# Optimization experiments

Hardware: AMD Instinct MI355X
Metric: run time of the kernel (lower is better)

The kernel has to match this reference:

```python
import jax, jax.numpy as jnp
import numpy as np

SIGMA = 0.01        # config['fscore_sigma']
FSCORE_W = 0.1      # config['fscore_weight']
TASK_W = 1.0        # config['task_weight']
DOMAIN_W = 0.1      # config['domain_weight']


def setup_inputs() -> dict:
    key = jax.random.key(0)
    ks = jax.random.split(key, 11)
    B, N, M, F = 8, 4096, 4096, 512
    H1, H2, D = 256, 128, 6
    return {
        "pred_pc": jax.random.normal(ks[0], (B, N, 3), jnp.float32),
        "target_pc": jax.random.normal(ks[1], (B, M, 3), jnp.float32),
        "domain_features": jax.random.normal(ks[2], (B, F), jnp.float32),
        "dataset_weights": jax.random.uniform(ks[3], (B,), jnp.float32, 0.9, 1.2),
        "W1": jax.random.normal(ks[4], (F, H1), jnp.float32) * 0.02,
        "b1": jnp.zeros((H1,), jnp.float32),
        "W2": jax.random.normal(ks[5], (H1, H2), jnp.float32) * 0.02,
        "b2": jnp.zeros((H2,), jnp.float32),
        "W3": jax.random.normal(ks[6], (H2, D), jnp.float32) * 0.02,
        "b3": jnp.zeros((D,), jnp.float32),
        "domain_labels": jax.random.randint(ks[7], (B,), 0, D),
    }


def _chamfer_mins(pred, tgt):
    # pred: [B,N,3], tgt: [B,M,3] -> squared pairwise dists [B,N,M], then dual mins
    d = (jnp.sum(pred ** 2, axis=2)[:, :, None]
         + jnp.sum(tgt ** 2, axis=2)[:, None, :]
         - 2.0 * jnp.einsum('bnd,bmd->bnm', pred, tgt))
    return jnp.min(d, axis=2), jnp.min(d, axis=1)   # [B,N], [B,M]


def reference(pred_pc, target_pc, domain_features, dataset_weights,
              W1, b1, W2, b2, W3, b3, domain_labels):
    min_a, min_b = _chamfer_mins(pred_pc, target_pc)
    c = 2.0 * SIGMA * SIGMA
    soft_a = jnp.exp(-min_a / c)
    soft_b = jnp.exp(-min_b / c)

    # batch-level task loss (compute_reconstruction_loss on full batch)
    chamfer = jnp.mean(min_a) + jnp.mean(min_b)
    prec = jnp.mean(soft_a)
    rec = jnp.mean(soft_b)
    fscore = 2.0 * prec * rec / (prec + rec + 1e-8)
    task = chamfer + FSCORE_W * (1.0 - fscore)

    # per-sample dataset-weighted loss (vectorized form of the Python loop)
    ch_i = jnp.mean(min_a, axis=1) + jnp.mean(min_b, axis=1)
    p_i = jnp.mean(soft_a, axis=1)
    r_i = jnp.mean(soft_b, axis=1)
    f_i = 2.0 * p_i * r_i / (p_i + r_i + 1e-8)
    loss_i = ch_i + FSCORE_W * (1.0 - f_i)
    dataset_weighted = jnp.mean(dataset_weights * loss_i)

    # domain loss: GRL is identity in forward; classifier in eval mode (dropout off)
    h = jax.nn.relu(domain_features @ W1 + b1)
    h = jax.nn.relu(h @ W2 + b2)
    logits = h @ W3 + b3
    logp = jax.nn.log_softmax(logits, axis=-1)
    domain = -jnp.mean(jnp.take_along_axis(logp, domain_labels[:, None], axis=1))

    total = TASK_W * task + DOMAIN_W * domain + dataset_weighted
    return total
```

## Files before the change

kernel.cpp:

```cpp
#include <hip/hip_runtime.h>
#include <math.h>

#define B 8
#define NPTS 4096
#define QPT 8
#define THREADS 256


template<int S, int LOG2S>
__global__ __launch_bounds__(THREADS, 4) void d1_kernel(
    const float* __restrict__ pred, const float* __restrict__ targ,
    const float* __restrict__ x, const float* __restrict__ W1,
    float* __restrict__ partial, float* __restrict__ sums32,
    float* __restrict__ h1p) {
  constexpr int REFS = NPTS / S;
  int id = blockIdx.x;
  int tid = threadIdx.x;

  __shared__ float4 refs[REFS];
  __shared__ float xs[64];

  if (id < 64) {
    if (id == 0 && tid < 32) sums32[tid] = 0.f;
    int b = id >> 3, kc = id & 7;
    if (tid < 64) xs[tid] = x[b * 512 + kc * 64 + tid];
    __syncthreads();
    float acc = 0.f;
    const float* w = W1 + (size_t)(kc * 64) * 256 + tid;
#pragma unroll 8
    for (int k = 0; k < 64; ++k) acc = fmaf(xs[k], w[k * 256], acc);
    h1p[(b * 8 + kc) * 256 + tid] = acc;
    return;
  }

  int cid = id - 64;
  int split  = cid & (S - 1);
  int qchunk = (cid >> LOG2S) & 1;
  int b      = (cid >> (LOG2S + 1)) & 7;
  int dir    = cid >> (LOG2S + 4);
  const float* qp = dir ? targ : pred;
  const float* rp = dir ? pred : targ;

  const float* rb = rp + ((size_t)b * NPTS + (size_t)split * REFS) * 3;
  for (int i = tid; i < REFS; i += THREADS) {
    float xx = rb[i * 3 + 0], yy = rb[i * 3 + 1], zz = rb[i * 3 + 2];
    refs[i] = make_float4(xx, yy, zz, 0.5f * (xx * xx + yy * yy + zz * zz));
  }
  __syncthreads();

  const float* qb = qp + (size_t)b * NPTS * 3;
  int q0 = qchunk * (QPT * THREADS) + tid;
  float qx[QPT], qy[QPT], qz[QPT], vmin[QPT];
#pragma unroll
  for (int i = 0; i < QPT; ++i) {
    int q = q0 + i * THREADS;
    qx[i] = qb[q * 3 + 0];
    qy[i] = qb[q * 3 + 1];
    qz[i] = qb[q * 3 + 2];
    vmin[i] = 3.4e38f;
  }

  for (int j = 0; j < REFS; j += 8) {
    float4 t[8];
#pragma unroll
    for (int u = 0; u < 8; ++u) t[u] = refs[j + u];
#pragma unroll
    for (int i = 0; i < QPT; ++i) {
      float s[8];
#pragma unroll
      for (int u = 0; u < 8; ++u)
        s[u] = fmaf(-qx[i], t[u].x,
               fmaf(-qy[i], t[u].y, fmaf(-qz[i], t[u].z, t[u].w)));
      float m01 = fminf(s[0], s[1]), m23 = fminf(s[2], s[3]);
      float m45 = fminf(s[4], s[5]), m67 = fminf(s[6], s[7]);
      vmin[i] = fminf(vmin[i],
                      fminf(fminf(m01, m23), fminf(m45, m67)));
    }
  }

  size_t base = (((size_t)dir * B + b) * S + split) * NPTS;
#pragma unroll
  for (int i = 0; i < QPT; ++i) {
    float qn = fmaf(qx[i], qx[i], fmaf(qy[i], qy[i], qz[i] * qz[i]));
    partial[base + q0 + i * THREADS] = fmaf(2.f, vmin[i], qn);
  }
}

template<int S>
__global__ __launch_bounds__(THREADS) void d2_kernel(
    const float* __restrict__ partial, float* __restrict__ sums32,
    const float* __restrict__ h1p, const float* __restrict__ b1,
    const float* __restrict__ W2, float* __restrict__ h2p) {
  int id = blockIdx.x;
  int tid = threadIdx.x;

  if (id >= 256) {
    int lid = id - 256;
    int b = lid >> 1, half = lid & 1;
    __shared__ float hs[128];
    if (tid < 128) {
      int k = half * 128 + tid;
      float a = b1[k];
#pragma unroll
      for (int p = 0; p < 8; ++p) a += h1p[(b * 8 + p) * 256 + k];
      hs[tid] = fmaxf(a, 0.f);
    }
    __syncthreads();
    if (tid < 128) {
      float acc = 0.f;
      const float* w = W2 + (size_t)(half * 128) * 128 + tid;
#pragma unroll 8
      for (int k = 0; k < 128; ++k) acc = fmaf(hs[k], w[k * 128], acc);
      h2p[(b * 2 + half) * 128 + tid] = acc;
    }
    return;
  }

  int chunk = id & 15;
  int b   = (id >> 4) & 7;
  int dir = id >> 7;
  size_t pb = ((size_t)dir * B + b) * S * NPTS;
  int q = chunk * 256 + tid;

  float m = 3.4e38f;
#pragma unroll
  for (int s = 0; s < S; ++s)
    m = fminf(m, partial[pb + (size_t)s * NPTS + q]);
  float s_min = m;
  float s_soft = __expf(-5000.0f * m);

  for (int off = 32; off > 0; off >>= 1) {
    s_min  += __shfl_down(s_min,  off);
    s_soft += __shfl_down(s_soft, off);
  }
  __shared__ float red[8];
  int wave = tid >> 6, lane = tid & 63;
  if (lane == 0) { red[wave * 2] = s_min; red[wave * 2 + 1] = s_soft; }
  __syncthreads();
  if (tid == 0) {
    float a = 0.f, c = 0.f;
    for (int w = 0; w < 4; ++w) { a += red[w * 2]; c += red[w * 2 + 1]; }
    atomicAdd(&sums32[(dir * B + b) * 2 + 0], a);
    atomicAdd(&sums32[(dir * B + b) * 2 + 1], c);
  }
}

__global__ __launch_bounds__(THREADS) void final_kernel(
    const float* __restrict__ h2p, const float* __restrict__ b2,
    const float* __restrict__ W3, const float* __restrict__ b3,
    const int* __restrict__ labels, const float* __restrict__ sums32,
    const float* __restrict__ w, float* __restrict__ out) {
  int tid = threadIdx.x;
  __shared__ float h2s[8 * 128];
  __shared__ float lg[48];
  __shared__ float nlls[8];

  for (int i = tid; i < 1024; i += THREADS) {
    int b = i >> 7, j = i & 127;
    float a = b2[j] + h2p[(b * 2 + 0) * 128 + j] + h2p[(b * 2 + 1) * 128 + j];
    h2s[i] = fmaxf(a, 0.f);
  }
  __syncthreads();
  if (tid < 48) {
    int b = tid / 6, d = tid % 6;
    float acc = b3[d];
#pragma unroll 8
    for (int k = 0; k < 128; ++k) acc = fmaf(h2s[b * 128 + k], W3[k * 6 + d], acc);
    lg[tid] = acc;
  }
  __syncthreads();
  if (tid < 8) {
    int b = tid;
    float mx = lg[b * 6];
    for (int d = 1; d < 6; ++d) mx = fmaxf(mx, lg[b * 6 + d]);
    float se = 0.f;
    for (int d = 0; d < 6; ++d) se += __expf(lg[b * 6 + d] - mx);
    int lab = labels[b];
    nlls[b] = -(lg[b * 6 + lab] - mx - __logf(se));
  }
  __syncthreads();
  if (tid == 0) {
    float chamfer = 0.f, prec = 0.f, rec = 0.f, dsw = 0.f, dom = 0.f;
    for (int b = 0; b < B; ++b) {
      float sa  = sums32[(0 * B + b) * 2 + 0];
      float ssa = sums32[(0 * B + b) * 2 + 1];
      float sb  = sums32[(1 * B + b) * 2 + 0];
      float ssb = sums32[(1 * B + b) * 2 + 1];
      float ma = sa / 4096.f, mb = sb / 4096.f;
      float p = ssa / 4096.f, r = ssb / 4096.f;
      chamfer += ma + mb;
      prec += p; rec += r;
      float f_i = 2.f * p * r / (p + r + 1e-8f);
      float loss_i = ma + mb + 0.1f * (1.f - f_i);
      dsw += w[b] * loss_i;
      dom += nlls[b];
    }
    chamfer *= (1.f / B); prec *= (1.f / B); rec *= (1.f / B);
    dsw *= (1.f / B); dom *= (1.f / B);
    float fscore = 2.f * prec * rec / (prec + rec + 1e-8f);
    float task = chamfer + 0.1f * (1.f - fscore);
    out[0] = 1.0f * task + 0.1f * dom + dsw;
  }
}

template<int S, int LOG2S>
static void run_pipeline(const float* pred, const float* targ, const float* x,
                         const float* wgt, const float* W1, const float* b1,
                         const float* W2, const float* b2, const float* W3,
                         const float* b3, const int* labels, float* out,
                         char* ws, hipStream_t stream) {
  float* partial = (float*)ws;
  float* sums32  = partial + (size_t)2 * B * S * NPTS;
  float* h1p     = sums32 + 32;
  float* h2p     = h1p + 64 * 256;

  hipLaunchKernelGGL((d1_kernel<S, LOG2S>), dim3(64 + 32 * S), dim3(THREADS),
                     0, stream, pred, targ, x, W1, partial, sums32, h1p);
  hipLaunchKernelGGL((d2_kernel<S>), dim3(256 + 16), dim3(THREADS), 0, stream,
                     partial, sums32, h1p, b1, W2, h2p);
  hipLaunchKernelGGL(final_kernel, dim3(1), dim3(THREADS), 0, stream,
                     h2p, b2, W3, b3, labels, sums32, wgt, out);
}

extern "C" void kernel_launch(void* const* d_in, const int* in_sizes, int n_in,
                              void* d_out, int out_size, void* d_ws, size_t ws_size,
                              hipStream_t stream) {
  const float* pred   = (const float*)d_in[0];
  const float* targ   = (const float*)d_in[1];
  const float* x      = (const float*)d_in[2];
  const float* wgt    = (const float*)d_in[3];
  const float* W1     = (const float*)d_in[4];
  const float* b1     = (const float*)d_in[5];
  const float* W2     = (const float*)d_in[6];
  const float* b2     = (const float*)d_in[7];
  const float* W3     = (const float*)d_in[8];
  const float* b3     = (const float*)d_in[9];
  const int*   labels = (const int*)d_in[10];
  float* out = (float*)d_out;
  char* ws = (char*)d_ws;

  auto need = [](int S) {
    return ((size_t)2 * B * S * NPTS + 32 + 64 * 256 + 16 * 128) * sizeof(float);
  };
  if (ws_size >= need(32))
    run_pipeline<32, 5>(pred, targ, x, wgt, W1, b1, W2, b2, W3, b3, labels,
                        out, ws, stream);
  else if (ws_size >= need(16))
    run_pipeline<16, 4>(pred, targ, x, wgt, W1, b1, W2, b2, W3, b3, labels,
                        out, ws, stream);
  else
    run_pipeline<8, 3>(pred, targ, x, wgt, W1, b1, W2, b2, W3, b3, labels,
                       out, ws, stream);
}
```

Baseline: 111.6 us.

## Fuse three-kernel pipeline into one cooperative persistent kernel with grid syncs

Merges the chamfer-min, reduction and classifier-head kernels into one cooperative kernel. Blocks loop over the old work ids, and grid.sync() replaces the kernel boundaries, which removes two launch gaps. The inner min tree now uses three-input min helpers, which may map to v_min3. Risks: the persistent grid (up to 1024 blocks) may leave the compute phase unbalanced, since 32*S work items are spread over fewer blocks. Grid sync has its own cost, and the extra shared memory may lower occupancy.

Measured after the change: 221.4 us. +98.3%, slower.

```diff
diff --git a/kernel.cpp b/kernel.cpp
--- a/kernel.cpp
+++ b/kernel.cpp
@@ -1,11 +1,213 @@
 #include <hip/hip_runtime.h>
+#include <hip/hip_cooperative_groups.h>
 #include <math.h>
+
+namespace cg = cooperative_groups;
 
 #define B 8
 #define NPTS 4096
 #define QPT 8
 #define THREADS 256
 
+__device__ __forceinline__ float min3f(float a, float b, float c) {
+  return fminf(fminf(a, b), c);
+}
+
+
+template<int S, int LOG2S>
+__global__ __launch_bounds__(THREADS, 4) void fused_kernel(
+    const float* __restrict__ pred, const float* __restrict__ targ,
+    const float* __restrict__ x, const float* __restrict__ W1,
+    const float* __restrict__ b1, const float* __restrict__ W2,
+    const float* __restrict__ b2, const float* __restrict__ W3,
+    const float* __restrict__ b3, const int* __restrict__ labels,
+    const float* __restrict__ wgt,
+    float* __restrict__ partial, float* __restrict__ sums32,
+    float* __restrict__ h1p, float* __restrict__ h2p,
+    float* __restrict__ out) {
+  constexpr int REFS = NPTS / S;
+  cg::grid_group grid = cg::this_grid();
+  const int tid = threadIdx.x;
+
+  __shared__ float4 refs[REFS];
+  __shared__ float xs[64];
+  __shared__ float hs[128];
+  __shared__ float red[8];
+  __shared__ float h2s[8 * 128];
+  __shared__ float lg[48];
+  __shared__ float nlls[8];
+
+  for (int id = blockIdx.x; id < 64; id += gridDim.x) {
+    if (id == 0 && tid < 32) sums32[tid] = 0.f;
+    int b = id >> 3, kc = id & 7;
+    if (tid < 64) xs[tid] = x[b * 512 + kc * 64 + tid];
+    __syncthreads();
+    float acc = 0.f;
+    const float* w = W1 + (size_t)(kc * 64) * 256 + tid;
+#pragma unroll 8
+    for (int k = 0; k < 64; ++k) acc = fmaf(xs[k], w[k * 256], acc);
+    h1p[(b * 8 + kc) * 256 + tid] = acc;
+    __syncthreads();
+  }
+
+  for (int cid = blockIdx.x; cid < 32 * S; cid += gridDim.x) {
+    int split  = cid & (S - 1);
+    int qchunk = (cid >> LOG2S) & 1;
+    int b      = (cid >> (LOG2S + 1)) & 7;
+    int dir    = cid >> (LOG2S + 4);
+    const float* qp = dir ? targ : pred;
+    const float* rp = dir ? pred : targ;
+
+    const float* rb = rp + ((size_t)b * NPTS + (size_t)split * REFS) * 3;
+    for (int i = tid; i < REFS; i += THREADS) {
+      float xx = rb[i * 3 + 0], yy = rb[i * 3 + 1], zz = rb[i * 3 + 2];
+      refs[i] = make_float4(xx, yy, zz, 0.5f * (xx * xx + yy * yy + zz * zz));
+    }
+    __syncthreads();
+
+    const float* qb = qp + (size_t)b * NPTS * 3;
+    int q0 = qchunk * (QPT * THREADS) + tid;
+    float qx[QPT], qy[QPT], qz[QPT], vmin[QPT];
+#pragma unroll
+    for (int i = 0; i < QPT; ++i) {
+      int q = q0 + i * THREADS;
+      qx[i] = qb[q * 3 + 0];
+      qy[i] = qb[q * 3 + 1];
+      qz[i] = qb[q * 3 + 2];
+      vmin[i] = 3.4e38f;
+    }
+
+    for (int j = 0; j < REFS; j += 8) {
+      float4 t[8];
+#pragma unroll
+      for (int u = 0; u < 8; ++u) t[u] = refs[j + u];
+#pragma unroll
+      for (int i = 0; i < QPT; ++i) {
+        float s[8];
+#pragma unroll
+        for (int u = 0; u < 8; ++u)
+          s[u] = fmaf(-qx[i], t[u].x,
+                 fmaf(-qy[i], t[u].y, fmaf(-qz[i], t[u].z, t[u].w)));
+        float m0 = min3f(s[0], s[1], s[2]);
+        float m1 = min3f(s[3], s[4], s[5]);
+        float m2 = min3f(s[6], s[7], m0);
+        vmin[i] = min3f(m1, m2, vmin[i]);
+      }
+    }
+
+    size_t base = (((size_t)dir * B + b) * S + split) * NPTS;
+#pragma unroll
+    for (int i = 0; i < QPT; ++i) {
+      float qn = fmaf(qx[i], qx[i], fmaf(qy[i], qy[i], qz[i] * qz[i]));
+      partial[base + q0 + i * THREADS] = fmaf(2.f, vmin[i], qn);
+    }
+    __syncthreads();
+  }
+
+  grid.sync();
+
+  for (int id = blockIdx.x; id < 272; id += gridDim.x) {
+    if (id >= 256) {
+      int lid = id - 256;
+      int b = lid >> 1, half = lid & 1;
+      if (tid < 128) {
+        int k = half * 128 + tid;
+        float a = b1[k];
+#pragma unroll
+        for (int p = 0; p < 8; ++p) a += h1p[(b * 8 + p) * 256 + k];
+        hs[tid] = fmaxf(a, 0.f);
+      }
+      __syncthreads();
+      if (tid < 128) {
+        float acc = 0.f;
+        const float* w = W2 + (size_t)(half * 128) * 128 + tid;
+#pragma unroll 8
+        for (int k = 0; k < 128; ++k) acc = fmaf(hs[k], w[k * 128], acc);
+        h2p[(b * 2 + half) * 128 + tid] = acc;
+      }
+      __syncthreads();
+    } else {
+      int chunk = id & 15;
+      int b   = (id >> 4) & 7;
+      int dir = id >> 7;
+      size_t pb = ((size_t)dir * B + b) * S * NPTS;
+      int q = chunk * 256 + tid;
+
+      float m = 3.4e38f;
+#pragma unroll
+      for (int s = 0; s < S; ++s)
+        m = fminf(m, partial[pb + (size_t)s * NPTS + q]);
+      float s_min = m;
+      float s_soft = __expf(-5000.0f * m);
+
+      for (int off = 32; off > 0; off >>= 1) {
+        s_min  += __shfl_down(s_min,  off);
+        s_soft += __shfl_down(s_soft, off);
+      }
+      int wave = tid >> 6, lane = tid & 63;
+      if (lane == 0) { red[wave * 2] = s_min; red[wave * 2 + 1] = s_soft; }
+      __syncthreads();
+      if (tid == 0) {
+        float a = 0.f, c = 0.f;
+        for (int wv = 0; wv < 4; ++wv) { a += red[wv * 2]; c += red[wv * 2 + 1]; }
+        atomicAdd(&sums32[(dir * B + b) * 2 + 0], a);
+        atomicAdd(&sums32[(dir * B + b) * 2 + 1], c);
+      }
+      __syncthreads();
+    }
+  }
+
+  grid.sync();
+
+  if (blockIdx.x == 0) {
+    for (int i = tid; i < 1024; i += THREADS) {
+      int b = i >> 7, j = i & 127;
+      float a = b2[j] + h2p[(b * 2 + 0) * 128 + j] + h2p[(b * 2 + 1) * 128 + j];
+      h2s[i] = fmaxf(a, 0.f);
+    }
+    __syncthreads();
+    if (tid < 48) {
+      int b = tid / 6, d = tid % 6;
+      float acc = b3[d];
+#pragma unroll 8
+      for (int k = 0; k < 128; ++k) acc = fmaf(h2s[b * 128 + k], W3[k * 6 + d], acc);
+      lg[tid] = acc;
+    }
+    __syncthreads();
+    if (tid < 8) {
+      int b = tid;
+      float mx = lg[b * 6];
+      for (int d = 1; d < 6; ++d) mx = fmaxf(mx, lg[b * 6 + d]);
+      float se = 0.f;
+      for (int d = 0; d < 6; ++d) se += __expf(lg[b * 6 + d] - mx);
+      int lab = labels[b];
+      nlls[b] = -(lg[b * 6 + lab] - mx - __logf(se));
+    }
+    __syncthreads();
+    if (tid == 0) {
+      float chamfer = 0.f, prec = 0.f, rec = 0.f, dsw = 0.f, dom = 0.f;
+      for (int b = 0; b < B; ++b) {
+        float sa  = sums32[(0 * B + b) * 2 + 0];
+        float ssa = sums32[(0 * B + b) * 2 + 1];
+        float sb  = sums32[(1 * B + b) * 2 + 0];
+        float ssb = sums32[(1 * B + b) * 2 + 1];
+        float ma = sa / 4096.f, mb = sb / 4096.f;
+        float p = ssa / 4096.f, r = ssb / 4096.f;
+        chamfer += ma + mb;
+        prec += p; rec += r;
+        float f_i = 2.f * p * r / (p + r + 1e-8f);
+        float loss_i = ma + mb + 0.1f * (1.f - f_i);
+        dsw += wgt[b] * loss_i;
+        dom += nlls[b];
+      }
+      chamfer *= (1.f / B); prec *= (1.f / B); rec *= (1.f / B);
+      dsw *= (1.f / B); dom *= (1.f / B);
+      float fscore = 2.f * prec * rec / (prec + rec + 1e-8f);
+      float task = chamfer + 0.1f * (1.f - fscore);
+      out[0] = 1.0f * task + 0.1f * dom + dsw;
+    }
+  }
+}
 
 template<int S, int LOG2S>
 __global__ __launch_bounds__(THREADS, 4) void d1_kernel(
@@ -71,10 +273,10 @@
       for (int u = 0; u < 8; ++u)
         s[u] = fmaf(-qx[i], t[u].x,
                fmaf(-qy[i], t[u].y, fmaf(-qz[i], t[u].z, t[u].w)));
-      float m01 = fminf(s[0], s[1]), m23 = fminf(s[2], s[3]);
-      float m45 = fminf(s[4], s[5]), m67 = fminf(s[6], s[7]);
-      vmin[i] = fminf(vmin[i],
-                      fminf(fminf(m01, m23), fminf(m45, m67)));
+      float m0 = min3f(s[0], s[1], s[2]);
+      float m1 = min3f(s[3], s[4], s[5]);
+      float m2 = min3f(s[6], s[7], m0);
+      vmin[i] = min3f(m1, m2, vmin[i]);
     }
   }
 
@@ -214,12 +416,43 @@
   float* h1p     = sums32 + 32;
   float* h2p     = h1p + 64 * 256;
 
-  hipLaunchKernelGGL((d1_kernel<S, LOG2S>), dim3(64 + 32 * S), dim3(THREADS),
-                     0, stream, pred, targ, x, W1, partial, sums32, h1p);
-  hipLaunchKernelGGL((d2_kernel<S>), dim3(256 + 16), dim3(THREADS), 0, stream,
-                     partial, sums32, h1p, b1, W2, h2p);
-  hipLaunchKernelGGL(final_kernel, dim3(1), dim3(THREADS), 0, stream,
-                     h2p, b2, W3, b3, labels, sums32, wgt, out);
+  static int g_blocks = 0;
+  if (g_blocks == 0) {
+    int dev = 0;
+    (void)hipGetDevice(&dev);
+    hipDeviceProp_t props;
+    int ncu = 256;
+    if (hipGetDeviceProperties(&props, dev) == hipSuccess &&
+        props.multiProcessorCount > 0)
+      ncu = props.multiProcessorCount;
+    int maxb = 0;
+    if (hipOccupancyMaxActiveBlocksPerMultiprocessor(
+            &maxb, fused_kernel<S, LOG2S>, THREADS, 0) != hipSuccess ||
+        maxb <= 0)
+      maxb = 2;
+    long g = (long)maxb * ncu;
+    if (g > 1024) g = 1024;
+    if (g < 64) g = 64;
+    g_blocks = (int)g;
+  }
+
+  void* args[] = {(void*)&pred, (void*)&targ, (void*)&x,    (void*)&W1,
+                  (void*)&b1,   (void*)&W2,   (void*)&b2,   (void*)&W3,
+                  (void*)&b3,   (void*)&labels, (void*)&wgt,
+                  (void*)&partial, (void*)&sums32, (void*)&h1p,
+                  (void*)&h2p,  (void*)&out};
+  hipError_t e = hipLaunchCooperativeKernel(fused_kernel<S, LOG2S>,
+                                            dim3(g_blocks), dim3(THREADS),
+                                            args, 0, stream);
+  if (e != hipSuccess) {
+    (void)hipGetLastError();
+    hipLaunchKernelGGL((d1_kernel<S, LOG2S>), dim3(64 + 32 * S), dim3(THREADS),
+                       0, stream, pred, targ, x, W1, partial, sums32, h1p);
+    hipLaunchKernelGGL((d2_kernel<S>), dim3(256 + 16), dim3(THREADS), 0, stream,
+                       partial, sums32, h1p, b1, W2, h2p);
+    hipLaunchKernelGGL(final_kernel, dim3(1), dim3(THREADS), 0, stream,
+                       h2p, b2, W3, b3, labels, sums32, wgt, out);
+  }
 }
 
 extern "C" void kernel_launch(void* const* d_in, const int* in_sizes, int n_in,
```

## Fuse final kernel via last-block pattern, SoA refs with packed FMA

Applied to the files above, without the earlier changes.

Removes the third launch: the d2-stage blocks count completions with an atomic, and the last block runs the domain MLP layers 2 and 3 plus the final loss. The MLP layer-1 blocks are folded into the first chamfer blocks instead of getting extra blocks. The reference points are stored as separate x/y/z/w arrays in shared memory, and the inner loop uses 2-wide vector FMAs and three-input mins so the compiler can emit packed math. The risks are a serialized tail in the last block, which computes the whole W2 layer alone, and a completion counter that is zeroed by k1 block 0 and so depends on stream ordering.

Result: slower. 137.4 us (+23.1%).

```diff
diff --git a/kernel.cpp b/kernel.cpp
--- a/kernel.cpp
+++ b/kernel.cpp
@@ -6,23 +6,47 @@
 #define QPT 8
 #define THREADS 256
 
+typedef float v2f __attribute__((ext_vector_type(2)));
+typedef float v4f __attribute__((ext_vector_type(4)));
+
+__device__ __forceinline__ float min3f(float a, float b, float c) {
+  return fminf(fminf(a, b), c);
+}
+
+#if __has_builtin(__builtin_elementwise_fma)
+__device__ __forceinline__ v2f fma2(v2f a, v2f b, v2f c) {
+  return __builtin_elementwise_fma(a, b, c);
+}
+#else
+__device__ __forceinline__ v2f fma2(v2f a, v2f b, v2f c) {
+  v2f r; r.x = __builtin_fmaf(a.x, b.x, c.x); r.y = __builtin_fmaf(a.y, b.y, c.y);
+  return r;
+}
+#endif
+
+#define VLO(v) __builtin_shufflevector(v, v, 0, 1)
+#define VHI(v) __builtin_shufflevector(v, v, 2, 3)
+
 
 template<int S, int LOG2S>
-__global__ __launch_bounds__(THREADS, 4) void d1_kernel(
+__global__ __launch_bounds__(THREADS, 4) void k1_kernel(
     const float* __restrict__ pred, const float* __restrict__ targ,
     const float* __restrict__ x, const float* __restrict__ W1,
-    float* __restrict__ partial, float* __restrict__ sums32,
+    float* __restrict__ partial, float* __restrict__ sums64,
     float* __restrict__ h1p) {
   constexpr int REFS = NPTS / S;
-  int id = blockIdx.x;
-  int tid = threadIdx.x;
-
-  __shared__ float4 refs[REFS];
+  const int tid = threadIdx.x;
+  const int cid = blockIdx.x;
+
+  __shared__ __align__(16) float sx[REFS];
+  __shared__ __align__(16) float sy[REFS];
+  __shared__ __align__(16) float sz[REFS];
+  __shared__ __align__(16) float sw[REFS];
   __shared__ float xs[64];
 
-  if (id < 64) {
-    if (id == 0 && tid < 32) sums32[tid] = 0.f;
-    int b = id >> 3, kc = id & 7;
+  if (cid < 64) {
+    if (cid == 0 && tid < 64) sums64[tid] = 0.f;
+    int b = cid >> 3, kc = cid & 7;
     if (tid < 64) xs[tid] = x[b * 512 + kc * 64 + tid];
     __syncthreads();
     float acc = 0.f;
@@ -30,10 +54,8 @@
 #pragma unroll 8
     for (int k = 0; k < 64; ++k) acc = fmaf(xs[k], w[k * 256], acc);
     h1p[(b * 8 + kc) * 256 + tid] = acc;
-    return;
-  }
-
-  int cid = id - 64;
+  }
+
   int split  = cid & (S - 1);
   int qchunk = (cid >> LOG2S) & 1;
   int b      = (cid >> (LOG2S + 1)) & 7;
@@ -44,7 +66,8 @@
   const float* rb = rp + ((size_t)b * NPTS + (size_t)split * REFS) * 3;
   for (int i = tid; i < REFS; i += THREADS) {
     float xx = rb[i * 3 + 0], yy = rb[i * 3 + 1], zz = rb[i * 3 + 2];
-    refs[i] = make_float4(xx, yy, zz, 0.5f * (xx * xx + yy * yy + zz * zz));
+    sx[i] = xx; sy[i] = yy; sz[i] = zz;
+    sw[i] = 0.5f * (xx * xx + yy * yy + zz * zz);
   }
   __syncthreads();
 
@@ -61,20 +84,27 @@
   }
 
   for (int j = 0; j < REFS; j += 8) {
-    float4 t[8];
-#pragma unroll
-    for (int u = 0; u < 8; ++u) t[u] = refs[j + u];
+    v4f xA = *(const v4f*)(sx + j), xB = *(const v4f*)(sx + j + 4);
+    v4f yA = *(const v4f*)(sy + j), yB = *(const v4f*)(sy + j + 4);
+    v4f zA = *(const v4f*)(sz + j), zB = *(const v4f*)(sz + j + 4);
+    v4f wA = *(const v4f*)(sw + j), wB = *(const v4f*)(sw + j + 4);
+    v2f x01 = VLO(xA), x23 = VHI(xA), x45 = VLO(xB), x67 = VHI(xB);
+    v2f y01 = VLO(yA), y23 = VHI(yA), y45 = VLO(yB), y67 = VHI(yB);
+    v2f z01 = VLO(zA), z23 = VHI(zA), z45 = VLO(zB), z67 = VHI(zB);
+    v2f w01 = VLO(wA), w23 = VHI(wA), w45 = VLO(wB), w67 = VHI(wB);
 #pragma unroll
     for (int i = 0; i < QPT; ++i) {
-      float s[8];
-#pragma unroll
-      for (int u = 0; u < 8; ++u)
-        s[u] = fmaf(-qx[i], t[u].x,
-               fmaf(-qy[i], t[u].y, fmaf(-qz[i], t[u].z, t[u].w)));
-      float m01 = fminf(s[0], s[1]), m23 = fminf(s[2], s[3]);
-      float m45 = fminf(s[4], s[5]), m67 = fminf(s[6], s[7]);
-      vmin[i] = fminf(vmin[i],
-                      fminf(fminf(m01, m23), fminf(m45, m67)));
+      v2f nx = {-qx[i], -qx[i]};
+      v2f ny = {-qy[i], -qy[i]};
+      v2f nz = {-qz[i], -qz[i]};
+      v2f s01 = fma2(nx, x01, fma2(ny, y01, fma2(nz, z01, w01)));
+      v2f s23 = fma2(nx, x23, fma2(ny, y23, fma2(nz, z23, w23)));
+      v2f s45 = fma2(nx, x45, fma2(ny, y45, fma2(nz, z45, w45)));
+      v2f s67 = fma2(nx, x67, fma2(ny, y67, fma2(nz, z67, w67)));
+      float m0 = min3f(s01.x, s01.y, s23.x);
+      float m1 = min3f(s23.y, s45.x, s45.y);
+      float m2 = min3f(s67.x, s67.y, m0);
+      vmin[i] = min3f(m1, m2, vmin[i]);
     }
   }
 
@@ -87,34 +117,17 @@
 }
 
 template<int S>
-__global__ __launch_bounds__(THREADS) void d2_kernel(
-    const float* __restrict__ partial, float* __restrict__ sums32,
+__global__ __launch_bounds__(THREADS) void k2_kernel(
+    const float* __restrict__ partial, float* __restrict__ sums64,
     const float* __restrict__ h1p, const float* __restrict__ b1,
-    const float* __restrict__ W2, float* __restrict__ h2p) {
-  int id = blockIdx.x;
-  int tid = threadIdx.x;
-
-  if (id >= 256) {
-    int lid = id - 256;
-    int b = lid >> 1, half = lid & 1;
-    __shared__ float hs[128];
-    if (tid < 128) {
-      int k = half * 128 + tid;
-      float a = b1[k];
-#pragma unroll
-      for (int p = 0; p < 8; ++p) a += h1p[(b * 8 + p) * 256 + k];
-      hs[tid] = fmaxf(a, 0.f);
-    }
-    __syncthreads();
-    if (tid < 128) {
-      float acc = 0.f;
-      const float* w = W2 + (size_t)(half * 128) * 128 + tid;
-#pragma unroll 8
-      for (int k = 0; k < 128; ++k) acc = fmaf(hs[k], w[k * 128], acc);
-      h2p[(b * 2 + half) * 128 + tid] = acc;
-    }
-    return;
-  }
+    const float* __restrict__ W2, const float* __restrict__ b2,
+    const float* __restrict__ W3, const float* __restrict__ b3,
+    const int* __restrict__ labels, const float* __restrict__ wgt,
+    float* __restrict__ out) {
+  const int id = blockIdx.x;
+  const int tid = threadIdx.x;
+  __shared__ float red[8];
+  __shared__ bool is_last;
 
   int chunk = id & 15;
   int b   = (id >> 4) & 7;
@@ -133,67 +146,80 @@
     s_min  += __shfl_down(s_min,  off);
     s_soft += __shfl_down(s_soft, off);
   }
-  __shared__ float red[8];
   int wave = tid >> 6, lane = tid & 63;
   if (lane == 0) { red[wave * 2] = s_min; red[wave * 2 + 1] = s_soft; }
   __syncthreads();
   if (tid == 0) {
     float a = 0.f, c = 0.f;
-    for (int w = 0; w < 4; ++w) { a += red[w * 2]; c += red[w * 2 + 1]; }
-    atomicAdd(&sums32[(dir * B + b) * 2 + 0], a);
-    atomicAdd(&sums32[(dir * B + b) * 2 + 1], c);
-  }
-}
-
-__global__ __launch_bounds__(THREADS) void final_kernel(
-    const float* __restrict__ h2p, const float* __restrict__ b2,
-    const float* __restrict__ W3, const float* __restrict__ b3,
-    const int* __restrict__ labels, const float* __restrict__ sums32,
-    const float* __restrict__ w, float* __restrict__ out) {
-  int tid = threadIdx.x;
+    for (int wv = 0; wv < 4; ++wv) { a += red[wv * 2]; c += red[wv * 2 + 1]; }
+    atomicAdd(&sums64[(dir * B + b) * 2 + 0], a);
+    atomicAdd(&sums64[(dir * B + b) * 2 + 1], c);
+    __threadfence();
+    unsigned t = atomicAdd((unsigned*)(sums64 + 32), 1u);
+    is_last = (t == 255u);
+  }
+  __syncthreads();
+  if (!is_last) return;
+  __threadfence();
+
+  __shared__ float h1s[8 * 256];
   __shared__ float h2s[8 * 128];
   __shared__ float lg[48];
   __shared__ float nlls[8];
 
+  for (int i = tid; i < 2048; i += THREADS) {
+    int bb = i >> 8, k = i & 255;
+    float a = b1[k];
+#pragma unroll
+    for (int p = 0; p < 8; ++p) a += h1p[(bb * 8 + p) * 256 + k];
+    h1s[i] = fmaxf(a, 0.f);
+  }
+  __syncthreads();
   for (int i = tid; i < 1024; i += THREADS) {
-    int b = i >> 7, j = i & 127;
-    float a = b2[j] + h2p[(b * 2 + 0) * 128 + j] + h2p[(b * 2 + 1) * 128 + j];
-    h2s[i] = fmaxf(a, 0.f);
+    int bb = i >> 7, jo = i & 127;
+    float acc = b2[jo];
+    const float* w2 = W2 + jo;
+    const float* h1r = h1s + bb * 256;
+#pragma unroll 8
+    for (int k = 0; k < 256; ++k) acc = fmaf(h1r[k], w2[(size_t)k * 128], acc);
+    h2s[i] = fmaxf(acc, 0.f);
   }
   __syncthreads();
   if (tid < 48) {
-    int b = tid / 6, d = tid % 6;
+    int bb = tid / 6, d = tid % 6;
     float acc = b3[d];
 #pragma unroll 8
-    for (int k = 0; k < 128; ++k) acc = fmaf(h2s[b * 128 + k], W3[k * 6 + d], acc);
+    for (int k = 0; k < 128; ++k)
+      acc = fmaf(h2s[bb * 128 + k], W3[k * 6 + d], acc);
     lg[tid] = acc;
   }
   __syncthreads();
   if (tid < 8) {
-    int b = tid;
-    float mx = lg[b * 6];
-    for (int d = 1; d < 6; ++d) mx = fmaxf(mx, lg[b * 6 + d]);
+    int bb = tid;
+    float mx = lg[bb * 6];
+    for (int d = 1; d < 6; ++d) mx = fmaxf(mx, lg[bb * 6 + d]);
     float se = 0.f;
-    for (int d = 0; d < 6; ++d) se += __expf(lg[b * 6 + d] - mx);
-    int lab = labels[b];
-    nlls[b] = -(lg[b * 6 + lab] - mx - __logf(se));
+    for (int d = 0; d < 6; ++d) se += __expf(lg[bb * 6 + d] - mx);
+    int lab = labels[bb];
+    nlls[bb] = -(lg[bb * 6 + lab] - mx - __logf(se));
   }
   __syncthreads();
   if (tid == 0) {
+    volatile const float* vs = (volatile const float*)sums64;
     float chamfer = 0.f, prec = 0.f, rec = 0.f, dsw = 0.f, dom = 0.f;
-    for (int b = 0; b < B; ++b) {
-      float sa  = sums32[(0 * B + b) * 2 + 0];
-      float ssa = sums32[(0 * B + b) * 2 + 1];
-      float sb  = sums32[(1 * B + b) * 2 + 0];
-      float ssb = sums32[(1 * B + b) * 2 + 1];
+    for (int bb = 0; bb < B; ++bb) {
+      float sa  = vs[(0 * B + bb) * 2 + 0];
+      float ssa = vs[(0 * B + bb) * 2 + 1];
+      float sb  = vs[(1 * B + bb) * 2 + 0];
+      float ssb = vs[(1 * B + bb) * 2 + 1];
       float ma = sa / 4096.f, mb = sb / 4096.f;
       float p = ssa / 4096.f, r = ssb / 4096.f;
       chamfer += ma + mb;
       prec += p; rec += r;
       float f_i = 2.f * p * r / (p + r + 1e-8f);
       float loss_i = ma + mb + 0.1f * (1.f - f_i);
-      dsw += w[b] * loss_i;
-      dom += nlls[b];
+      dsw += wgt[bb] * loss_i;
+      dom += nlls[bb];
     }
     chamfer *= (1.f / B); prec *= (1.f / B); rec *= (1.f / B);
     dsw *= (1.f / B); dom *= (1.f / B);
@@ -210,16 +236,14 @@
                          const float* b3, const int* labels, float* out,
                          char* ws, hipStream_t stream) {
   float* partial = (float*)ws;
-  float* sums32  = partial + (size_t)2 * B * S * NPTS;
-  float* h1p     = sums32 + 32;
-  float* h2p     = h1p + 64 * 256;
-
-  hipLaunchKernelGGL((d1_kernel<S, LOG2S>), dim3(64 + 32 * S), dim3(THREADS),
-                     0, stream, pred, targ, x, W1, partial, sums32, h1p);
-  hipLaunchKernelGGL((d2_kernel<S>), dim3(256 + 16), dim3(THREADS), 0, stream,
-                     partial, sums32, h1p, b1, W2, h2p);
-  hipLaunchKernelGGL(final_kernel, dim3(1), dim3(THREADS), 0, stream,
-                     h2p, b2, W3, b3, labels, sums32, wgt, out);
+  float* sums64  = partial + (size_t)2 * B * S * NPTS;
+  float* h1p     = sums64 + 64;
+
+  hipLaunchKernelGGL((k1_kernel<S, LOG2S>), dim3(32 * S), dim3(THREADS),
+                     0, stream, pred, targ, x, W1, partial, sums64, h1p);
+  hipLaunchKernelGGL((k2_kernel<S>), dim3(256), dim3(THREADS), 0, stream,
+                     partial, sums64, h1p, b1, W2, b2, W3, b3, labels, wgt,
+                     out);
 }
 
 extern "C" void kernel_launch(void* const* d_in, const int* in_sizes, int n_in,
@@ -240,7 +264,7 @@
   char* ws = (char*)d_ws;
 
   auto need = [](int S) {
-    return ((size_t)2 * B * S * NPTS + 32 + 64 * 256 + 16 * 128) * sizeof(float);
+    return ((size_t)2 * B * S * NPTS + 64 + 64 * 256) * sizeof(float);
   };
   if (ws_size >= need(32))
     run_pipeline<32, 5>(pred, targ, x, wgt, W1, b1, W2, b2, W3, b3, labels,
```
